# Optimization experiments

Measured on AMD Instinct MI355X. Metric: run time of the kernel, lower is better.

Reference implementation:

```python
import jax, jax.numpy as jnp
import numpy as np

D_MODEL = 256
D_STATE = 64
D_CONV = 4
EXPAND = 2
HEADDIM = 64
D_INNER = EXPAND * D_MODEL          # 512
NHEADS = D_INNER // HEADDIM         # 8
CONV_DIM = D_INNER + 2 * D_STATE    # 640
D_IN_PROJ = 2 * D_INNER + 2 * D_STATE + NHEADS  # 1160
BATCH = 4
SEQ = 4096  # H*W = 64*64


def _silu(x):
    return x * jax.nn.sigmoid(x)


def _layernorm(x, w, b, eps=1e-5):
    mu = jnp.mean(x, axis=-1, keepdims=True)
    xc = x - mu
    var = jnp.mean(xc * xc, axis=-1, keepdims=True)
    return xc * jax.lax.rsqrt(var + eps) * w + b


def _mamba2(x, W_in, conv_w, conv_b, dt_bias, A_log, D_param, rms_w, W_out):
    # x: (B, L, d_model)
    B, L, _ = x.shape
    zxbcdt = x @ W_in.T                                   # (B,L,1160)
    z = zxbcdt[..., :D_INNER]                             # gate (B,L,512)
    xBC = zxbcdt[..., D_INNER:D_INNER + CONV_DIM]         # (B,L,640)
    dt = jax.nn.softplus(zxbcdt[..., -NHEADS:] + dt_bias) # (B,L,8)
    # causal depthwise conv (kernel D_CONV) + SiLU
    xp = jnp.pad(xBC, ((0, 0), (D_CONV - 1, 0), (0, 0)))
    xBC = sum(xp[:, k:k + L, :] * conv_w[:, k] for k in range(D_CONV)) + conv_b
    xBC = _silu(xBC)
    xh = xBC[..., :D_INNER].reshape(B, L, NHEADS, HEADDIM)
    Bm = xBC[..., D_INNER:D_INNER + D_STATE]              # (B,L,64), ngroups=1
    Cm = xBC[..., D_INNER + D_STATE:]                     # (B,L,64)
    dA = jnp.exp(dt * (-jnp.exp(A_log)))                  # (B,L,H) decay per head

    def step(h, ins):
        # h: (B,H,P,N)
        dA_t, dt_t, x_t, B_t, C_t = ins
        h = dA_t[:, :, None, None] * h + jnp.einsum('bh,bhp,bn->bhpn', dt_t, x_t, B_t)
        y = jnp.einsum('bhpn,bn->bhp', h, C_t)
        return h, y

    h0 = jnp.zeros((B, NHEADS, HEADDIM, D_STATE), x.dtype)
    _, ys = jax.lax.scan(step, h0, (jnp.swapaxes(dA, 0, 1), jnp.swapaxes(dt, 0, 1),
                                    jnp.swapaxes(xh, 0, 1), jnp.swapaxes(Bm, 0, 1),
                                    jnp.swapaxes(Cm, 0, 1)))
    y = jnp.swapaxes(ys, 0, 1) + D_param[:, None] * xh    # skip term, (B,L,H,P)
    y = y.reshape(B, L, D_INNER) * _silu(z)               # gated
    y = y * jax.lax.rsqrt(jnp.mean(y * y, axis=-1, keepdims=True) + 1e-5) * rms_w
    return y @ W_out.T


def setup_inputs() -> dict:
    key = jax.random.key(0)
    ks = jax.random.split(key, 10)
    s = 0.02
    return {
        'x0_seq': jax.random.normal(ks[0], (BATCH, SEQ, D_MODEL), jnp.float32),
        'x1_seq': jax.random.normal(ks[1], (BATCH, SEQ, D_MODEL), jnp.float32),
        'norm_s_w': jnp.ones((D_MODEL,), jnp.float32),
        'norm_s_b': jnp.zeros((D_MODEL,), jnp.float32),
        'W_in': jax.random.normal(ks[2], (D_IN_PROJ, D_MODEL), jnp.float32) * s,
        'conv_w': jax.random.normal(ks[3], (CONV_DIM, D_CONV), jnp.float32) * 0.2,
        'conv_b': jnp.zeros((CONV_DIM,), jnp.float32),
        'dt_bias': jax.random.normal(ks[4], (NHEADS,), jnp.float32) * 0.1,
        'A_log': jnp.log(jnp.arange(1, NHEADS + 1, dtype=jnp.float32)),
        'D_param': jnp.ones((NHEADS,), jnp.float32),
        'rms_w': jnp.ones((D_INNER,), jnp.float32),
        'W_out': jax.random.normal(ks[5], (D_MODEL, D_INNER), jnp.float32) * s,
        'mlp_w1': jax.random.normal(ks[6], (D_MODEL, 2 * D_MODEL), jnp.float32) * s,
        'mlp_b1': jnp.zeros((D_MODEL,), jnp.float32),
        'mlp_w2': jax.random.normal(ks[7], (D_MODEL, D_MODEL), jnp.float32) * s,
        'mlp_b2': jnp.zeros((D_MODEL,), jnp.float32),
        'norm_t_w': jnp.ones((D_MODEL,), jnp.float32),
        'norm_t_b': jnp.zeros((D_MODEL,), jnp.float32),
        'H': 64,
        'W': 64,
    }


def reference(x0_seq, x1_seq, norm_s_w, norm_s_b, W_in, conv_w, conv_b, dt_bias,
              A_log, D_param, rms_w, W_out, mlp_w1, mlp_b1, mlp_w2, mlp_b2,
              norm_t_w, norm_t_b, H, W):
    B = x0_seq.shape[0]
    x_cat = jnp.concatenate([x0_seq, x1_seq], axis=0)     # (2B,L,C)
    x_norm = _layernorm(x_cat, norm_s_w, norm_s_b)
    sp = _mamba2(x_norm, W_in, conv_w, conv_b, dt_bias, A_log, D_param, rms_w, W_out) + x_cat
    f0, f1 = sp[:B], sp[B:]

    def mlp(a, b):
        h = _silu(jnp.concatenate([a, b], axis=-1) @ mlp_w1.T + mlp_b1)
        return h @ mlp_w2.T + mlp_b2

    f0_fused = _layernorm(f0 + mlp(f0, f1), norm_t_w, norm_t_b)
    f1_fused = _layernorm(f1 + mlp(f1, f0), norm_t_w, norm_t_b)
    return (f0_fused, f1_fused)
```

## Files before the change

kernel.cpp:

```cpp
#include <hip/hip_runtime.h>
#include <math.h>

typedef unsigned short bf16_t;
typedef __attribute__((ext_vector_type(8))) short bf16x8;
typedef __attribute__((ext_vector_type(4))) float f32x4;

#define LSEQ 4096
#define NTOK 32768
#define HALF_TOK 16384
#define TPAD 72

__device__ __forceinline__ float bf2f(bf16_t u) {
    unsigned int x = ((unsigned int)u) << 16;
    return __uint_as_float(x);
}
__device__ __forceinline__ bf16_t f2bf(float f) {
    unsigned int x = __float_as_uint(f);
    unsigned int r = (x + 0x7FFFu + ((x >> 16) & 1u)) >> 16;
    return (bf16_t)r;
}
__device__ __forceinline__ float siluf(float x) { return x / (1.f + __expf(-x)); }

__device__ __forceinline__ void unpack8(uint4 u, float* f) {
    f[0] = bf2f((bf16_t)(u.x & 0xffff)); f[1] = bf2f((bf16_t)(u.x >> 16));
    f[2] = bf2f((bf16_t)(u.y & 0xffff)); f[3] = bf2f((bf16_t)(u.y >> 16));
    f[4] = bf2f((bf16_t)(u.z & 0xffff)); f[5] = bf2f((bf16_t)(u.z >> 16));
    f[6] = bf2f((bf16_t)(u.w & 0xffff)); f[7] = bf2f((bf16_t)(u.w >> 16));
}
__device__ __forceinline__ uint4 pack8(const float* f) {
    uint4 u;
    u.x = (unsigned)f2bf(f[0]) | ((unsigned)f2bf(f[1]) << 16);
    u.y = (unsigned)f2bf(f[2]) | ((unsigned)f2bf(f[3]) << 16);
    u.z = (unsigned)f2bf(f[4]) | ((unsigned)f2bf(f[5]) << 16);
    u.w = (unsigned)f2bf(f[6]) | ((unsigned)f2bf(f[7]) << 16);
    return u;
}
__device__ __forceinline__ void st4(bf16_t* p, const float* o) {
    ushort4 u; u.x = f2bf(o[0]); u.y = f2bf(o[1]); u.z = f2bf(o[2]); u.w = f2bf(o[3]);
    *(ushort4*)p = u;
}

__device__ __forceinline__ void gload16(const bf16_t* g, bf16_t* l) {
    __builtin_amdgcn_global_load_lds(
        (const __attribute__((address_space(1))) unsigned int*)g,
        (__attribute__((address_space(3))) unsigned int*)l,
        16, 0, 0);
}

__device__ __forceinline__ void stage_N(bf16_t (*T)[TPAD], const bf16_t* g, int rs, int tid) {
    #pragma unroll
    for (int it = 0; it < 2; ++it) {
        int slot = it * 256 + tid;
        int r = slot >> 3, co = slot & 7;
        *(uint4*)&T[r][co * 8] = *(const uint4*)(g + (size_t)r * rs + co * 8);
    }
}

__device__ __forceinline__ void stage_T(bf16_t (*T)[TPAD], const bf16_t* g, int rs, int tid) {
    int rp = tid >> 3;
    int co = tid & 7;
    int r0 = rp * 2;
    const bf16_t* p0 = g + (size_t)r0 * rs + co * 8;
    uint4 a = *(const uint4*)p0;
    uint4 b = *(const uint4*)(p0 + rs);
    unsigned aa[4] = {a.x, a.y, a.z, a.w};
    unsigned bb[4] = {b.x, b.y, b.z, b.w};
    #pragma unroll
    for (int q = 0; q < 4; ++q) {
        int c0 = co * 8 + q * 2;
        *(unsigned*)&T[c0][r0]     = (aa[q] & 0xffffu) | (bb[q] << 16 & 0xffff0000u);
        *(unsigned*)&T[c0 + 1][r0] = (aa[q] >> 16)     | (bb[q] & 0xffff0000u);
    }
}

__global__ __launch_bounds__(256) void wconv_kernel(
    const float* __restrict__ s, bf16_t* __restrict__ d, int n4)
{
    int i = blockIdx.x * 256 + threadIdx.x;
    if (i < n4) {
        float4 v = ((const float4*)s)[i];
        ushort4 u; u.x = f2bf(v.x); u.y = f2bf(v.y); u.z = f2bf(v.z); u.w = f2bf(v.w);
        ((ushort4*)d)[i] = u;
    }
}

__global__ __launch_bounds__(256) void ln_cat_kernel(
    const float* __restrict__ x0, const float* __restrict__ x1,
    const float* __restrict__ w, const float* __restrict__ b,
    bf16_t* __restrict__ out)
{
    int row = blockIdx.x * 4 + (threadIdx.x >> 6);
    int lane = threadIdx.x & 63;
    const float* src = (row < HALF_TOK) ? x0 + (size_t)row * 256
                                        : x1 + (size_t)(row - HALF_TOK) * 256;
    float4 v = ((const float4*)src)[lane];
    float s = v.x + v.y + v.z + v.w;
    float sq = v.x*v.x + v.y*v.y + v.z*v.z + v.w*v.w;
    #pragma unroll
    for (int off = 32; off; off >>= 1) { s += __shfl_xor(s, off); sq += __shfl_xor(sq, off); }
    float mu = s * (1.f/256.f);
    float var = sq * (1.f/256.f) - mu*mu;
    float inv = rsqrtf(var + 1e-5f);
    float4 wv = ((const float4*)w)[lane];
    float4 bv = ((const float4*)b)[lane];
    float o[4];
    o[0] = (v.x-mu)*inv*wv.x + bv.x;
    o[1] = (v.y-mu)*inv*wv.y + bv.y;
    o[2] = (v.z-mu)*inv*wv.z + bv.z;
    o[3] = (v.w-mu)*inv*wv.w + bv.w;
    st4(out + (size_t)row * 256 + lane * 4, o);
}

template<int AMODE, typename TC, bool BIAS, bool SILU, bool RES, bool DUAL>
__global__ __launch_bounds__(256) void gemm_mfma(
    const bf16_t* __restrict__ A, const bf16_t* __restrict__ W,
    const float* __restrict__ bias, TC* __restrict__ C,
    const float* __restrict__ r0, const float* __restrict__ r1,
    bf16_t* __restrict__ C2,
    int M, int N, int K)
{
    __shared__ bf16_t As[128 * 64];
    __shared__ bf16_t Ws[128 * 64];
    const int tid = threadIdx.x;
    const int wave = tid >> 6, lane = tid & 63;
    const int m0 = blockIdx.x << 7, n0 = blockIdx.y << 7;
    const int wr = wave >> 1, wc = wave & 1;
    const int fr = lane & 15, fk = lane >> 4;

    const int srow = lane >> 3;
    const int schunk = (lane & 7) ^ srow;

    f32x4 acc[4][4] = {};

    for (int k0 = 0; k0 < K; k0 += 64) {
        __syncthreads();
        #pragma unroll
        for (int t = 0; t < 4; ++t) {
            int row = wave * 32 + t * 8 + srow;
            const bf16_t* ga;
            if (AMODE == 0) {
                ga = A + (size_t)(m0 + row) * K + k0 + schunk * 8;
            } else {
                int m = m0 + row;
                if (k0 < 256) ga = A + (size_t)m * 256 + k0 + schunk * 8;
                else          ga = A + (size_t)(m ^ HALF_TOK) * 256 + (k0 - 256) + schunk * 8;
            }
            gload16(ga, As + wave * 2048 + t * 512);
            const bf16_t* gw = W + (size_t)(n0 + row) * K + k0 + schunk * 8;
            gload16(gw, Ws + wave * 2048 + t * 512);
        }
        __syncthreads();

        #pragma unroll
        for (int half = 0; half < 2; ++half) {
            bf16x8 af[4], bfr[4];
            #pragma unroll
            for (int i = 0; i < 4; ++i) {
                int row = wr * 64 + i * 16 + fr;
                int c16 = (half * 4 + fk) ^ (row & 7);
                af[i] = *(const bf16x8*)&As[row * 64 + c16 * 8];
            }
            #pragma unroll
            for (int j = 0; j < 4; ++j) {
                int row = wc * 64 + j * 16 + fr;
                int c16 = (half * 4 + fk) ^ (row & 7);
                bfr[j] = *(const bf16x8*)&Ws[row * 64 + c16 * 8];
            }
            #pragma unroll
            for (int i = 0; i < 4; ++i)
                #pragma unroll
                for (int j = 0; j < 4; ++j)
                    acc[i][j] = __builtin_amdgcn_mfma_f32_16x16x32_bf16(af[i], bfr[j], acc[i][j], 0, 0, 0);
        }
    }

    int fq = lane >> 4;
    #pragma unroll
    for (int j = 0; j < 4; ++j) {
        int n = n0 + wc * 64 + j * 16 + fr;
        if (n >= N) continue;
        float bval = BIAS ? bias[n] : 0.f;
        #pragma unroll
        for (int i = 0; i < 4; ++i) {
            #pragma unroll
            for (int q = 0; q < 4; ++q) {
                int m = m0 + wr * 64 + i * 16 + fq * 4 + q;
                float v = acc[i][j][q];
                if (BIAS) v += bval;
                if (SILU) v = siluf(v);
                if (RES) v += (m < HALF_TOK) ? r0[(size_t)m * 256 + n]
                                             : r1[(size_t)(m - HALF_TOK) * 256 + n];
                if (sizeof(TC) == 4) ((float*)C)[(size_t)m * N + n] = v;
                else ((bf16_t*)C)[(size_t)m * N + n] = f2bf(v);
                if (DUAL) C2[(size_t)m * N + n] = f2bf(v);
            }
        }
    }
}

__global__ __launch_bounds__(320) void conv_dt_kernel(
    const bf16_t* __restrict__ zx, const float* __restrict__ cw,
    const float* __restrict__ cb, const float* __restrict__ dtb,
    const float* __restrict__ alog,
    bf16_t* __restrict__ conv_out, float* __restrict__ dts, float* __restrict__ lda)
{
    int tl = threadIdx.x / 80;
    int slot = threadIdx.x - tl * 80;
    int tok = blockIdx.x * 4 + tl;
    int b = tok >> 12, t = tok & 4095;
    int ch = slot * 8;

    float f[4][8];
    #pragma unroll
    for (int k = 0; k < 4; ++k) {
        int tp = t - 3 + k;
        if (tp >= 0) {
            uint4 u = *(const uint4*)(zx + (size_t)(b * LSEQ + tp) * 1160 + 512 + ch);
            unpack8(u, f[k]);
        } else {
            #pragma unroll
            for (int j = 0; j < 8; ++j) f[k][j] = 0.f;
        }
    }
    float o[8];
    #pragma unroll
    for (int j = 0; j < 8; ++j) {
        float4 w4 = *(const float4*)(cw + (ch + j) * 4);
        float acc = cb[ch + j] + w4.x * f[0][j] + w4.y * f[1][j] + w4.z * f[2][j] + w4.w * f[3][j];
        o[j] = siluf(acc);
    }
    *(uint4*)(conv_out + (size_t)tok * 640 + ch) = pack8(o);

    if (slot < 8) {
        int h = slot;
        float raw = bf2f(zx[(size_t)tok * 1160 + 1152 + h]) + dtb[h];
        float dt = (raw > 20.f) ? raw : log1pf(__expf(raw));
        dts[tok * 8 + h] = dt;
        lda[tok * 8 + h] = -dt * __expf(alog[h]);
    }
}

__global__ __launch_bounds__(256) void scan_passA(
    const bf16_t* __restrict__ conv_out, const float* __restrict__ dts,
    const float* __restrict__ lda, bf16_t* __restrict__ SH, float* __restrict__ Dtot)
{
    int bh = blockIdx.x, c = blockIdx.y;
    int b = bh >> 3, h = bh & 7;
    __shared__ bf16_t Xt[64][TPAD];
    __shared__ bf16_t Bw[64][TPAD];
    __shared__ float wls[64];
    int tid = threadIdx.x;
    int tokbase = b * LSEQ + c * 64;

    if (tid < 64) {
        float la = lda[(tokbase + tid) * 8 + h];
        #pragma unroll
        for (int off = 1; off < 64; off <<= 1) {
            float up = __shfl_up(la, off);
            if (tid >= off) la += up;
        }
        float tot = __shfl(la, 63);
        wls[tid] = __expf(tot - la) * dts[(tokbase + tid) * 8 + h];
        if (tid == 63) Dtot[bh * 64 + c] = __expf(tot);
    }
    stage_T(Xt, conv_out + (size_t)tokbase * 640 + h * 64, 640, tid);
    __syncthreads();

    {
        int rp = tid >> 3, co = tid & 7;
        int r0 = rp * 2;
        const bf16_t* p0 = conv_out + (size_t)(tokbase + r0) * 640 + 512 + co * 8;
        uint4 a = *(const uint4*)p0;
        uint4 bq = *(const uint4*)(p0 + 640);
        float fa[8], fb[8];
        unpack8(a, fa); unpack8(bq, fb);
        float w0 = wls[r0], w1 = wls[r0 + 1];
        #pragma unroll
        for (int q = 0; q < 8; ++q) {
            int c0 = co * 8 + q;
            *(unsigned*)&Bw[c0][r0] =
                (unsigned)f2bf(fa[q] * w0) | ((unsigned)f2bf(fb[q] * w1) << 16);
        }
    }
    __syncthreads();

    int wv = tid >> 6, lane = tid & 63;
    int fr = lane & 15, fk = lane >> 4;
    f32x4 acc[4] = {};
    bf16x8 af0 = *(const bf16x8*)&Xt[wv * 16 + fr][fk * 8];
    bf16x8 af1 = *(const bf16x8*)&Xt[wv * 16 + fr][32 + fk * 8];
    #pragma unroll
    for (int j = 0; j < 4; ++j) {
        bf16x8 b0 = *(const bf16x8*)&Bw[j * 16 + fr][fk * 8];
        bf16x8 b1 = *(const bf16x8*)&Bw[j * 16 + fr][32 + fk * 8];
        acc[j] = __builtin_amdgcn_mfma_f32_16x16x32_bf16(af0, b0, acc[j], 0, 0, 0);
        acc[j] = __builtin_amdgcn_mfma_f32_16x16x32_bf16(af1, b1, acc[j], 0, 0, 0);
    }
    __syncthreads();
    #pragma unroll
    for (int j = 0; j < 4; ++j)
        #pragma unroll
        for (int q = 0; q < 4; ++q) {
            int p = wv * 16 + fk * 4 + q;
            Xt[p][j * 16 + fr] = f2bf(acc[j][q]);
        }
    __syncthreads();
    size_t base = (size_t)(bh * 64 + c) * 4096;
    #pragma unroll
    for (int it = 0; it < 2; ++it) {
        int slot = it * 256 + tid;
        int p = slot >> 3, co = slot & 7;
        *(uint4*)(SH + base + p * 64 + co * 8) = *(const uint4*)&Xt[p][co * 8];
    }
}

__global__ __launch_bounds__(256) void scan_passB(bf16_t* __restrict__ SH, const float* __restrict__ Dtot)
{
    int bh = blockIdx.x;
    int elem = blockIdx.y * 256 + threadIdx.x;
    size_t base = (size_t)bh * 64 * 4096 + elem;
    float H = 0.f;
    for (int c = 0; c < 64; ++c) {
        float d = Dtot[bh * 64 + c];
        size_t a = base + (size_t)c * 4096;
        float s = bf2f(SH[a]);
        SH[a] = f2bf(H);
        H = d * H + s;
    }
}

__global__ __launch_bounds__(256) void scan_passC(
    const bf16_t* __restrict__ conv_out, const float* __restrict__ dts,
    const float* __restrict__ lda, const bf16_t* __restrict__ SH,
    bf16_t* __restrict__ ybuf)
{
    int bh = blockIdx.x, c = blockIdx.y;
    int b = bh >> 3, h = bh & 7;
    __shared__ bf16_t Cs[64][TPAD];
    __shared__ bf16_t Bs[64][TPAD];
    __shared__ bf16_t Hs[64][TPAD];
    __shared__ bf16_t Xt[64][TPAD];
    __shared__ float La_sh[64], dt_sh[64], ce_sh[64];
    int tid = threadIdx.x;
    int tokbase = b * LSEQ + c * 64;
    size_t shbase = (size_t)(bh * 64 + c) * 4096;

    if (tid < 64) {
        float la = lda[(tokbase + tid) * 8 + h];
        #pragma unroll
        for (int off = 1; off < 64; off <<= 1) {
            float up = __shfl_up(la, off);
            if (tid >= off) la += up;
        }
        La_sh[tid] = la;
        ce_sh[tid] = __expf(la);
        dt_sh[tid] = dts[(tokbase + tid) * 8 + h];
    }
    stage_N(Cs, conv_out + (size_t)tokbase * 640 + 576, 640, tid);
    stage_N(Bs, conv_out + (size_t)tokbase * 640 + 512, 640, tid);
    stage_N(Hs, SH + shbase, 64, tid);
    stage_T(Xt, conv_out + (size_t)tokbase * 640 + h * 64, 640, tid);
    __syncthreads();

    int wv = tid >> 6, lane = tid & 63;
    int fr = lane & 15, fk = lane >> 4;
    int ws = wv * 16;

    bf16x8 afC0 = *(const bf16x8*)&Cs[ws + fr][fk * 8];
    bf16x8 afC1 = *(const bf16x8*)&Cs[ws + fr][32 + fk * 8];
    f32x4 accG[4] = {}, accH[4] = {};
    #pragma unroll
    for (int j = 0; j < 4; ++j) {
        bf16x8 b0 = *(const bf16x8*)&Bs[j * 16 + fr][fk * 8];
        bf16x8 b1 = *(const bf16x8*)&Bs[j * 16 + fr][32 + fk * 8];
        accG[j] = __builtin_amdgcn_mfma_f32_16x16x32_bf16(afC0, b0, accG[j], 0, 0, 0);
        accG[j] = __builtin_amdgcn_mfma_f32_16x16x32_bf16(afC1, b1, accG[j], 0, 0, 0);
        bf16x8 h0 = *(const bf16x8*)&Hs[j * 16 + fr][fk * 8];
        bf16x8 h1 = *(const bf16x8*)&Hs[j * 16 + fr][32 + fk * 8];
        accH[j] = __builtin_amdgcn_mfma_f32_16x16x32_bf16(afC0, h0, accH[j], 0, 0, 0);
        accH[j] = __builtin_amdgcn_mfma_f32_16x16x32_bf16(afC1, h1, accH[j], 0, 0, 0);
    }

    #pragma unroll
    for (int j = 0; j < 4; ++j)
        #pragma unroll
        for (int q = 0; q < 4; ++q) {
            int s = ws + fk * 4 + q;
            int r = j * 16 + fr;
            float m1 = 0.f;
            if (r <= s) m1 = accG[j][q] * __expf(La_sh[s] - La_sh[r]) * dt_sh[r];
            Cs[s][r] = f2bf(m1);
        }
    #pragma unroll
    for (int j = 0; j < 4; ++j)
        #pragma unroll
        for (int q = 0; q < 4; ++q)
            accH[j][q] *= ce_sh[ws + fk * 4 + q];

    bf16x8 afM0 = *(const bf16x8*)&Cs[ws + fr][fk * 8];
    bf16x8 afM1 = *(const bf16x8*)&Cs[ws + fr][32 + fk * 8];
    #pragma unroll
    for (int j = 0; j < 4; ++j) {
        bf16x8 x0 = *(const bf16x8*)&Xt[j * 16 + fr][fk * 8];
        bf16x8 x1 = *(const bf16x8*)&Xt[j * 16 + fr][32 + fk * 8];
        accH[j] = __builtin_amdgcn_mfma_f32_16x16x32_bf16(afM0, x0, accH[j], 0, 0, 0);
        accH[j] = __builtin_amdgcn_mfma_f32_16x16x32_bf16(afM1, x1, accH[j], 0, 0, 0);
    }

    __syncthreads();
    #pragma unroll
    for (int j = 0; j < 4; ++j)
        #pragma unroll
        for (int q = 0; q < 4; ++q) {
            int s = ws + fk * 4 + q;
            Bs[s][j * 16 + fr] = f2bf(accH[j][q]);
        }
    __syncthreads();
    #pragma unroll
    for (int it = 0; it < 2; ++it) {
        int slot = it * 256 + tid;
        int r = slot >> 3, co = slot & 7;
        *(uint4*)(ybuf + (size_t)(tokbase + r) * 512 + h * 64 + co * 8) = *(const uint4*)&Bs[r][co * 8];
    }
}

__global__ __launch_bounds__(256) void gate_rms_kernel(
    bf16_t* __restrict__ y, const bf16_t* __restrict__ conv_out,
    const bf16_t* __restrict__ zx, const float* __restrict__ Dp,
    const float* __restrict__ rw)
{
    int row = blockIdx.x * 4 + (threadIdx.x >> 6);
    int lane = threadIdx.x & 63;
    uint4* yrow = (uint4*)(y + (size_t)row * 512);
    uint4 uy = yrow[lane];
    uint4 ux = *(const uint4*)(conv_out + (size_t)row * 640 + lane * 8);
    uint4 uz = *(const uint4*)(zx + (size_t)row * 1160 + lane * 8);
    float fy[8], fx[8], fz[8];
    unpack8(uy, fy); unpack8(ux, fx); unpack8(uz, fz);
    float d = Dp[lane >> 3];
    float v[8];
    float sq = 0.f;
    #pragma unroll
    for (int i = 0; i < 8; ++i) {
        v[i] = (fy[i] + d * fx[i]) * siluf(fz[i]);
        sq += v[i] * v[i];
    }
    #pragma unroll
    for (int off = 32; off; off >>= 1) sq += __shfl_xor(sq, off);
    float r = rsqrtf(sq * (1.f/512.f) + 1e-5f);
    float4 w0 = *(const float4*)(rw + lane * 8);
    float4 w1 = *(const float4*)(rw + lane * 8 + 4);
    float o[8];
    o[0] = v[0]*r*w0.x; o[1] = v[1]*r*w0.y; o[2] = v[2]*r*w0.z; o[3] = v[3]*r*w0.w;
    o[4] = v[4]*r*w1.x; o[5] = v[5]*r*w1.y; o[6] = v[6]*r*w1.z; o[7] = v[7]*r*w1.w;
    yrow[lane] = pack8(o);
}

__global__ __launch_bounds__(256) void final_ln_kernel(
    const float* __restrict__ sp, const float* __restrict__ mo,
    const float* __restrict__ w, const float* __restrict__ b,
    float* __restrict__ out)
{
    int row = blockIdx.x * 4 + (threadIdx.x >> 6);
    int lane = threadIdx.x & 63;
    float4 a = ((const float4*)(sp + (size_t)row * 256))[lane];
    float4 c = ((const float4*)(mo + (size_t)row * 256))[lane];
    float4 v = {a.x + c.x, a.y + c.y, a.z + c.z, a.w + c.w};
    float s = v.x + v.y + v.z + v.w;
    float sq = v.x*v.x + v.y*v.y + v.z*v.z + v.w*v.w;
    #pragma unroll
    for (int off = 32; off; off >>= 1) { s += __shfl_xor(s, off); sq += __shfl_xor(sq, off); }
    float mu = s * (1.f/256.f);
    float var = sq * (1.f/256.f) - mu*mu;
    float inv = rsqrtf(var + 1e-5f);
    float4 wv = ((const float4*)w)[lane];
    float4 bv = ((const float4*)b)[lane];
    float4 o;
    o.x = (v.x-mu)*inv*wv.x + bv.x;
    o.y = (v.y-mu)*inv*wv.y + bv.y;
    o.z = (v.z-mu)*inv*wv.z + bv.z;
    o.w = (v.w-mu)*inv*wv.w + bv.w;
    ((float4*)(out + (size_t)row * 256))[lane] = o;
}

extern "C" void kernel_launch(void* const* d_in, const int* in_sizes, int n_in,
                              void* d_out, int out_size, void* d_ws, size_t ws_size,
                              hipStream_t stream) {
    (void)in_sizes; (void)n_in; (void)out_size; (void)ws_size;
    const float* x0      = (const float*)d_in[0];
    const float* x1      = (const float*)d_in[1];
    const float* nsw     = (const float*)d_in[2];
    const float* nsb     = (const float*)d_in[3];
    const float* W_in    = (const float*)d_in[4];
    const float* conv_w  = (const float*)d_in[5];
    const float* conv_b  = (const float*)d_in[6];
    const float* dt_bias = (const float*)d_in[7];
    const float* A_log   = (const float*)d_in[8];
    const float* D_param = (const float*)d_in[9];
    const float* rms_w   = (const float*)d_in[10];
    const float* W_out   = (const float*)d_in[11];
    const float* mlp_w1  = (const float*)d_in[12];
    const float* mlp_b1  = (const float*)d_in[13];
    const float* mlp_w2  = (const float*)d_in[14];
    const float* mlp_b2  = (const float*)d_in[15];
    const float* ntw     = (const float*)d_in[16];
    const float* ntb     = (const float*)d_in[17];
    float* out = (float*)d_out;

    char* base = (char*)d_ws;
    bf16_t* zx = (bf16_t*)base;
    float*  sp = (float*)base;
    char* pB = base + 76021760;
    bf16_t* convo = (bf16_t*)pB;
    bf16_t* hbuf  = (bf16_t*)pB;
    char* pC = pB + 41943040;
    bf16_t* x_norm = (bf16_t*)pC;
    bf16_t* SH     = (bf16_t*)pC;
    bf16_t* spb    = (bf16_t*)pC;
    char* pD = pC + 33554432;
    bf16_t* ybuf = (bf16_t*)pD;
    float*  mout = (float*)pD;
    char* pE = pD + 33554432;
    float* dts  = (float*)pE;
    float* lda  = dts + 262144;
    float* dtot = lda + 262144;
    bf16_t* Wb_in = (bf16_t*)(dtot + 4096);
    bf16_t* Wb_o  = Wb_in + 296960;
    bf16_t* Wb_1  = Wb_o + 131072;
    bf16_t* Wb_2  = Wb_1 + 131072;

    wconv_kernel<<<(74240 + 255) / 256, 256, 0, stream>>>(W_in,   Wb_in, 74240);
    wconv_kernel<<<(32768 + 255) / 256, 256, 0, stream>>>(W_out,  Wb_o,  32768);
    wconv_kernel<<<(32768 + 255) / 256, 256, 0, stream>>>(mlp_w1, Wb_1,  32768);
    wconv_kernel<<<(16384 + 255) / 256, 256, 0, stream>>>(mlp_w2, Wb_2,  16384);

    ln_cat_kernel<<<8192, 256, 0, stream>>>(x0, x1, nsw, nsb, x_norm);

    dim3 g_in(256, 10);
    gemm_mfma<0, bf16_t, false, false, false, false><<<g_in, 256, 0, stream>>>(
        x_norm, Wb_in, nullptr, zx, nullptr, nullptr, nullptr, NTOK, 1160, 256);

    conv_dt_kernel<<<8192, 320, 0, stream>>>(zx, conv_w, conv_b, dt_bias, A_log, convo, dts, lda);

    dim3 g_scan(64, 64);
    scan_passA<<<g_scan, 256, 0, stream>>>(convo, dts, lda, SH, dtot);
    dim3 g_pb(64, 16);
    scan_passB<<<g_pb, 256, 0, stream>>>(SH, dtot);
    scan_passC<<<g_scan, 256, 0, stream>>>(convo, dts, lda, SH, ybuf);

    gate_rms_kernel<<<8192, 256, 0, stream>>>(ybuf, convo, zx, D_param, rms_w);

    dim3 g_out(256, 2);
    gemm_mfma<0, float, false, false, true, true><<<g_out, 256, 0, stream>>>(
        ybuf, Wb_o, nullptr, sp, x0, x1, spb, NTOK, 256, 512);

    gemm_mfma<1, bf16_t, true, true, false, false><<<g_out, 256, 0, stream>>>(
        spb, Wb_1, mlp_b1, hbuf, nullptr, nullptr, nullptr, NTOK, 256, 512);

    gemm_mfma<0, float, true, false, false, false><<<g_out, 256, 0, stream>>>(
        hbuf, Wb_2, mlp_b2, mout, nullptr, nullptr, nullptr, NTOK, 256, 256);

    final_ln_kernel<<<8192, 256, 0, stream>>>(sp, mout, ntw, ntb, out);
}
```

Before: 397.7 us.

## Fuse second MLP GEMM with final LayerNorm; reuse conv window across tokens

Adds an mlp2_ln_kernel that computes the second MLP GEMM across a full 256-wide row tile per block, adds bias and the residual, and applies the final LayerNorm in registers using cross-lane reductions. This removes the fp32 intermediate write and read of the MLP output and one kernel launch. Separately, the conv kernel now handles 4 consecutive tokens per thread and reuses a 7-row sliding window, which cuts redundant global loads. The risks are the larger accumulator register footprint (32 f32x4 per thread), which can lower occupancy, and a grid of only 256 blocks for the fused GEMM.

```diff
diff --git a/kernel.cpp b/kernel.cpp
--- a/kernel.cpp
+++ b/kernel.cpp
@@ -198,6 +198,100 @@
     }
 }
 
+__global__ __launch_bounds__(256) void mlp2_ln_kernel(
+    const bf16_t* __restrict__ A, const bf16_t* __restrict__ W,
+    const float* __restrict__ bias, const float* __restrict__ sp,
+    const float* __restrict__ lnw, const float* __restrict__ lnb,
+    float* __restrict__ out)
+{
+    __shared__ bf16_t As[128 * 64];
+    __shared__ bf16_t Ws[256 * 64];
+    const int tid = threadIdx.x;
+    const int wave = tid >> 6, lane = tid & 63;
+    const int m0 = blockIdx.x << 7;
+    const int fr = lane & 15, fk = lane >> 4;
+    const int srow = lane >> 3;
+    const int schunk = (lane & 7) ^ srow;
+
+    f32x4 acc[2][16] = {};
+
+    for (int k0 = 0; k0 < 256; k0 += 64) {
+        __syncthreads();
+        #pragma unroll
+        for (int t = 0; t < 4; ++t) {
+            int row = wave * 32 + t * 8 + srow;
+            gload16(A + (size_t)(m0 + row) * 256 + k0 + schunk * 8, As + wave * 2048 + t * 512);
+        }
+        #pragma unroll
+        for (int t = 0; t < 8; ++t) {
+            int row = wave * 64 + t * 8 + srow;
+            gload16(W + (size_t)row * 256 + k0 + schunk * 8, Ws + wave * 4096 + t * 512);
+        }
+        __syncthreads();
+
+        #pragma unroll
+        for (int half = 0; half < 2; ++half) {
+            bf16x8 af[2];
+            #pragma unroll
+            for (int i = 0; i < 2; ++i) {
+                int row = wave * 32 + i * 16 + fr;
+                int c16 = (half * 4 + fk) ^ (row & 7);
+                af[i] = *(const bf16x8*)&As[row * 64 + c16 * 8];
+            }
+            #pragma unroll
+            for (int j = 0; j < 16; ++j) {
+                int row = j * 16 + fr;
+                int c16 = (half * 4 + fk) ^ (row & 7);
+                bf16x8 bfr = *(const bf16x8*)&Ws[row * 64 + c16 * 8];
+                acc[0][j] = __builtin_amdgcn_mfma_f32_16x16x32_bf16(af[0], bfr, acc[0][j], 0, 0, 0);
+                acc[1][j] = __builtin_amdgcn_mfma_f32_16x16x32_bf16(af[1], bfr, acc[1][j], 0, 0, 0);
+            }
+        }
+    }
+
+    float s1[2][4] = {}, s2[2][4] = {};
+    #pragma unroll
+    for (int i = 0; i < 2; ++i)
+        #pragma unroll
+        for (int j = 0; j < 16; ++j) {
+            int n = j * 16 + fr;
+            float bv = bias[n];
+            #pragma unroll
+            for (int q = 0; q < 4; ++q) {
+                int m = m0 + wave * 32 + i * 16 + fk * 4 + q;
+                float v = acc[i][j][q] + bv + sp[(size_t)m * 256 + n];
+                acc[i][j][q] = v;
+                s1[i][q] += v;
+                s2[i][q] += v * v;
+            }
+        }
+    #pragma unroll
+    for (int i = 0; i < 2; ++i)
+        #pragma unroll
+        for (int q = 0; q < 4; ++q) {
+            float a = s1[i][q], b2 = s2[i][q];
+            #pragma unroll
+            for (int off = 8; off; off >>= 1) {
+                a  += __shfl_xor(a,  off);
+                b2 += __shfl_xor(b2, off);
+            }
+            s1[i][q] = a * (1.f/256.f);
+            s2[i][q] = rsqrtf(b2 * (1.f/256.f) - s1[i][q]*s1[i][q] + 1e-5f);
+        }
+    #pragma unroll
+    for (int i = 0; i < 2; ++i)
+        #pragma unroll
+        for (int j = 0; j < 16; ++j) {
+            int n = j * 16 + fr;
+            float wv = lnw[n], bv = lnb[n];
+            #pragma unroll
+            for (int q = 0; q < 4; ++q) {
+                int m = m0 + wave * 32 + i * 16 + fk * 4 + q;
+                out[(size_t)m * 256 + n] = (acc[i][j][q] - s1[i][q]) * s2[i][q] * wv + bv;
+            }
+        }
+}
+
 __global__ __launch_bounds__(320) void conv_dt_kernel(
     const bf16_t* __restrict__ zx, const float* __restrict__ cw,
     const float* __restrict__ cb, const float* __restrict__ dtb,
@@ -206,37 +300,52 @@
 {
     int tl = threadIdx.x / 80;
     int slot = threadIdx.x - tl * 80;
-    int tok = blockIdx.x * 4 + tl;
-    int b = tok >> 12, t = tok & 4095;
+    int tok0 = blockIdx.x * 16 + tl * 4;
+    int b = tok0 >> 12, t0 = tok0 & 4095;
     int ch = slot * 8;
 
-    float f[4][8];
-    #pragma unroll
-    for (int k = 0; k < 4; ++k) {
-        int tp = t - 3 + k;
+    const bf16_t* basep = zx + (size_t)b * LSEQ * 1160 + 512 + ch;
+    float f[7][8];
+    #pragma unroll
+    for (int i = 0; i < 7; ++i) {
+        int tp = t0 - 3 + i;
         if (tp >= 0) {
-            uint4 u = *(const uint4*)(zx + (size_t)(b * LSEQ + tp) * 1160 + 512 + ch);
-            unpack8(u, f[k]);
+            uint4 u = *(const uint4*)(basep + (size_t)tp * 1160);
+            unpack8(u, f[i]);
         } else {
             #pragma unroll
-            for (int j = 0; j < 8; ++j) f[k][j] = 0.f;
-        }
-    }
-    float o[8];
+            for (int j = 0; j < 8; ++j) f[i][j] = 0.f;
+        }
+    }
+    float4 w4[8];
+    float cbv[8];
     #pragma unroll
     for (int j = 0; j < 8; ++j) {
-        float4 w4 = *(const float4*)(cw + (ch + j) * 4);
-        float acc = cb[ch + j] + w4.x * f[0][j] + w4.y * f[1][j] + w4.z * f[2][j] + w4.w * f[3][j];
-        o[j] = siluf(acc);
-    }
-    *(uint4*)(conv_out + (size_t)tok * 640 + ch) = pack8(o);
+        w4[j] = *(const float4*)(cw + (ch + j) * 4);
+        cbv[j] = cb[ch + j];
+    }
+    #pragma unroll
+    for (int d = 0; d < 4; ++d) {
+        float o[8];
+        #pragma unroll
+        for (int j = 0; j < 8; ++j) {
+            float a = cbv[j] + w4[j].x * f[d][j] + w4[j].y * f[d+1][j]
+                             + w4[j].z * f[d+2][j] + w4[j].w * f[d+3][j];
+            o[j] = siluf(a);
+        }
+        *(uint4*)(conv_out + (size_t)(tok0 + d) * 640 + ch) = pack8(o);
+    }
 
     if (slot < 8) {
         int h = slot;
-        float raw = bf2f(zx[(size_t)tok * 1160 + 1152 + h]) + dtb[h];
-        float dt = (raw > 20.f) ? raw : log1pf(__expf(raw));
-        dts[tok * 8 + h] = dt;
-        lda[tok * 8 + h] = -dt * __expf(alog[h]);
+        #pragma unroll
+        for (int d = 0; d < 4; ++d) {
+            int tok = tok0 + d;
+            float raw = bf2f(zx[(size_t)tok * 1160 + 1152 + h]) + dtb[h];
+            float dt = (raw > 20.f) ? raw : log1pf(__expf(raw));
+            dts[tok * 8 + h] = dt;
+            lda[tok * 8 + h] = -dt * __expf(alog[h]);
+        }
     }
 }
 
@@ -454,33 +563,6 @@
     o[0] = v[0]*r*w0.x; o[1] = v[1]*r*w0.y; o[2] = v[2]*r*w0.z; o[3] = v[3]*r*w0.w;
     o[4] = v[4]*r*w1.x; o[5] = v[5]*r*w1.y; o[6] = v[6]*r*w1.z; o[7] = v[7]*r*w1.w;
     yrow[lane] = pack8(o);
-}
-
-__global__ __launch_bounds__(256) void final_ln_kernel(
-    const float* __restrict__ sp, const float* __restrict__ mo,
-    const float* __restrict__ w, const float* __restrict__ b,
-    float* __restrict__ out)
-{
-    int row = blockIdx.x * 4 + (threadIdx.x >> 6);
-    int lane = threadIdx.x & 63;
-    float4 a = ((const float4*)(sp + (size_t)row * 256))[lane];
-    float4 c = ((const float4*)(mo + (size_t)row * 256))[lane];
-    float4 v = {a.x + c.x, a.y + c.y, a.z + c.z, a.w + c.w};
-    float s = v.x + v.y + v.z + v.w;
-    float sq = v.x*v.x + v.y*v.y + v.z*v.z + v.w*v.w;
-    #pragma unroll
-    for (int off = 32; off; off >>= 1) { s += __shfl_xor(s, off); sq += __shfl_xor(sq, off); }
-    float mu = s * (1.f/256.f);
-    float var = sq * (1.f/256.f) - mu*mu;
-    float inv = rsqrtf(var + 1e-5f);
-    float4 wv = ((const float4*)w)[lane];
-    float4 bv = ((const float4*)b)[lane];
-    float4 o;
-    o.x = (v.x-mu)*inv*wv.x + bv.x;
-    o.y = (v.y-mu)*inv*wv.y + bv.y;
-    o.z = (v.z-mu)*inv*wv.z + bv.z;
-    o.w = (v.w-mu)*inv*wv.w + bv.w;
-    ((float4*)(out + (size_t)row * 256))[lane] = o;
 }
 
 extern "C" void kernel_launch(void* const* d_in, const int* in_sizes, int n_in,
@@ -519,7 +601,6 @@
     bf16_t* spb    = (bf16_t*)pC;
     char* pD = pC + 33554432;
     bf16_t* ybuf = (bf16_t*)pD;
-    float*  mout = (float*)pD;
     char* pE = pD + 33554432;
     float* dts  = (float*)pE;
     float* lda  = dts + 262144;
@@ -540,7 +621,7 @@
     gemm_mfma<0, bf16_t, false, false, false, false><<<g_in, 256, 0, stream>>>(
         x_norm, Wb_in, nullptr, zx, nullptr, nullptr, nullptr, NTOK, 1160, 256);
 
-    conv_dt_kernel<<<8192, 320, 0, stream>>>(zx, conv_w, conv_b, dt_bias, A_log, convo, dts, lda);
+    conv_dt_kernel<<<2048, 320, 0, stream>>>(zx, conv_w, conv_b, dt_bias, A_log, convo, dts, lda);
 
     dim3 g_scan(64, 64);
     scan_passA<<<g_scan, 256, 0, stream>>>(convo, dts, lda, SH, dtot);
@@ -557,8 +638,5 @@
     gemm_mfma<1, bf16_t, true, true, false, false><<<g_out, 256, 0, stream>>>(
         spb, Wb_1, mlp_b1, hbuf, nullptr, nullptr, nullptr, NTOK, 256, 512);
 
-    gemm_mfma<0, float, true, false, false, false><<<g_out, 256, 0, stream>>>(
-        hbuf, Wb_2, mlp_b2, mout, nullptr, nullptr, nullptr, NTOK, 256, 256);
-
-    final_ln_kernel<<<8192, 256, 0, stream>>>(sp, mout, ntw, ntb, out);
-}
+    mlp2_ln_kernel<<<256, 256, 0, stream>>>(hbuf, Wb_2, mlp_b2, sp, ntw, ntb, out);
+}
```

Result: faster. 375.5 us (-5.6%).
